# Kernel tuning notes

Hardware: AMD Instinct MI355X
Metric: run time of the kernel (lower is better)

The kernel has to match this reference:

```python
import jax, jax.numpy as jnp
import numpy as np

K = 512   # codebook entries per group (num_embeddings // 4)
D = 128   # dim per group (embedding_dim // 4)
BETA = 0.25


def setup_inputs() -> dict:
    key = jax.random.key(0)
    k0, k1, k2, k3, k4 = jax.random.split(key, 5)
    latents = jax.random.normal(k0, (16, 2048, 512), dtype=jnp.float32)
    scale = 1.0 / K
    w1 = jax.random.uniform(k1, (K, D), dtype=jnp.float32, minval=-scale, maxval=scale)
    w2 = jax.random.uniform(k2, (K, D), dtype=jnp.float32, minval=-scale, maxval=scale)
    w3 = jax.random.uniform(k3, (K, D), dtype=jnp.float32, minval=-scale, maxval=scale)
    w4 = jax.random.uniform(k4, (K, D), dtype=jnp.float32, minval=-scale, maxval=scale)
    return {"latents": latents, "w1": w1, "w2": w2, "w3": w3, "w4": w4}


def _vq(latents, w1, w2, w3, w4):
    B, S, E = latents.shape
    # Slicing [:, :, g*D:(g+1)*D] is equivalent to reshape into groups.
    x = latents.reshape(B, S, 4, D)                    # [B,S,4,D]
    W = jnp.stack([w1, w2, w3, w4], axis=0)            # [4,K,D]
    x_sq = jnp.sum(x * x, axis=-1, keepdims=True)      # [B,S,4,1]
    w_sq = jnp.sum(W * W, axis=-1)                     # [4,K]
    cross = jnp.einsum('bsgd,gkd->bsgk', x, W)         # [B,S,4,K]
    dist = x_sq + w_sq[None, None, :, :] - 2.0 * cross
    idx = jnp.argmin(dist, axis=-1)                    # [B,S,4]
    g_idx = jnp.arange(4)[None, None, :]
    q = W[g_idx, idx]                                  # [B,S,4,D]
    # per-group MSE losses (mean over B,S,D)
    sg = jax.lax.stop_gradient
    commit = jnp.mean((sg(q) - x) ** 2, axis=(0, 1, 3))   # [4]
    embed = jnp.mean((q - sg(x)) ** 2, axis=(0, 1, 3))    # [4]
    vq_loss = jnp.sum(BETA * commit + embed)
    # straight-through estimator
    q_st = x + sg(q - x)
    return q_st.reshape(B, S, E), vq_loss


def reference(latents, w1, w2, w3, w4):
    return _vq(latents, w1, w2, w3, w4)
```

## Files before the change

kernel.cpp:

```cpp
#include <hip/hip_runtime.h>
#include <stdint.h>

typedef __attribute__((ext_vector_type(8))) short short8;
typedef __attribute__((ext_vector_type(4))) float f32x4;

#define BIG 4.0f

static __device__ __forceinline__ short f2bf(float f) {
    union { float f; uint32_t u; } v; v.f = f;
    uint32_t u = v.u;
    return (short)((u + 0x7FFFu + ((u >> 16) & 1u)) >> 16);
}

static __device__ __forceinline__ void gload_lds16(const void* g, void* l) {
    __builtin_amdgcn_global_load_lds(
        (const __attribute__((address_space(1))) unsigned int*)g,
        (__attribute__((address_space(3))) unsigned int*)l, 16, 0, 0);
}


__global__ void vq_prep_kernel(const float* __restrict__ w0, const float* __restrict__ w1,
                               const float* __restrict__ w2, const float* __restrict__ w3,
                               float* __restrict__ ws) {
    int tid = blockIdx.x * 256 + threadIdx.x;
    int code = tid >> 4;
    int u    = tid & 15;
    int g = code >> 9, c = code & 511;
    int nt = c >> 4, lr = c & 15, ks = u >> 2, lh = u & 3;
    const float* wg = (g == 0) ? w0 : (g == 1) ? w1 : (g == 2) ? w2 : w3;
    const float* src = wg + (size_t)c * 128 + u * 8;
    float4 v0 = *(const float4*)(src);
    float4 v1 = *(const float4*)(src + 4);
    float s = v0.x*v0.x + v0.y*v0.y + v0.z*v0.z + v0.w*v0.w
            + v1.x*v1.x + v1.y*v1.y + v1.z*v1.z + v1.w*v1.w;
    short8 b;
    b[0] = f2bf(v0.x); b[1] = f2bf(v0.y); b[2] = f2bf(v0.z); b[3] = f2bf(v0.w);
    b[4] = f2bf(v1.x); b[5] = f2bf(v1.y); b[6] = f2bf(v1.z); b[7] = f2bf(v1.w);
    char* cb = (char*)ws + 65536 + (size_t)g * 131072;
    *(short8*)(cb + (size_t)(((nt * 4 + ks) * 64 + lh * 16 + lr) * 16)) = b;
    s += __shfl_xor(s, 1); s += __shfl_xor(s, 2);
    s += __shfl_xor(s, 4); s += __shfl_xor(s, 8);
    if (u == 0) ws[64 + code] = BIG - 0.5f * s;
}

__global__ __launch_bounds__(512, 2)
void vq_main_kernel(const float* __restrict__ lat,
                    const float* __restrict__ w0, const float* __restrict__ w1,
                    const float* __restrict__ w2, const float* __restrict__ w3,
                    float* __restrict__ out, float* __restrict__ ws) {
    __shared__ __align__(16) short lw[65536];
    __shared__ float lwsq[512];
    __shared__ float slsum[8];

    const int bid   = blockIdx.x;
    const int g     = bid >> 6;
    const int tbase = (bid & 63) * 512;
    const float* wg = (g == 0) ? w0 : (g == 1) ? w1 : (g == 2) ? w2 : w3;
    const char* cbg = (const char*)ws + 65536 + (size_t)g * 131072;

    const int t    = threadIdx.x;
    const int wave = t >> 6;
    const int l    = t & 63;
    const int lr   = l & 15;
    const int lh   = l >> 4;
    const uint32_t invlr = 511 - lr;

    lwsq[t] = ws[64 + g * 512 + t];

    {
        const char* gsrc = cbg + wave * 16384 + l * 16;
        char* ldst = (char*)lw + wave * 16384;
        #pragma unroll
        for (int j = 0; j < 16; j++)
            gload_lds16(gsrc + j * 1024, ldst + j * 1024);
    }

    auto load_convert = [&](short8 (&fr)[2][4], float (&xsp)[2], int wt) {
        #pragma unroll
        for (int mt = 0; mt < 2; mt++) {
            int token = wt + mt * 16 + lr;
            const float* xp = lat + (size_t)token * 512 + g * 128 + lh * 8;
            float part = 0.f;
            #pragma unroll
            for (int ks = 0; ks < 4; ks++) {
                float4 v0 = *(const float4*)(xp + ks * 32);
                float4 v1 = *(const float4*)(xp + ks * 32 + 4);
                part += v0.x*v0.x + v0.y*v0.y + v0.z*v0.z + v0.w*v0.w
                      + v1.x*v1.x + v1.y*v1.y + v1.z*v1.z + v1.w*v1.w;
                short8 a;
                a[0] = f2bf(v0.x); a[1] = f2bf(v0.y); a[2] = f2bf(v0.z); a[3] = f2bf(v0.w);
                a[4] = f2bf(v1.x); a[5] = f2bf(v1.y); a[6] = f2bf(v1.z); a[7] = f2bf(v1.w);
                fr[mt][ks] = a;
            }
            part += __shfl_xor(part, 16);
            part += __shfl_xor(part, 32);
            xsp[mt] = part;
        }
    };

    const char* lwb = (const char*)lw + l * 16;

    auto compute = [&](short8 (&af)[2][4], uint32_t (&rk)[8]) {
        short8 p0 = *(const short8*)(lwb);
        short8 p1 = *(const short8*)(lwb + 1024);
        short8 p2 = *(const short8*)(lwb + 2048);
        short8 p3 = *(const short8*)(lwb + 3072);
        float  ph = lwsq[lr];
        #pragma unroll 4
        for (int nt = 0; nt < 32; nt++) {
            short8 c0 = p0, c1 = p1, c2 = p2, c3 = p3;
            float  hn = ph;
            const char* nb = lwb + ((nt + 1) & 31) * 4096;
            p0 = *(const short8*)(nb);
            p1 = *(const short8*)(nb + 1024);
            p2 = *(const short8*)(nb + 2048);
            p3 = *(const short8*)(nb + 3072);
            ph = lwsq[(((nt + 1) & 31) << 4) + lr];
            const uint32_t invc = invlr - (uint32_t)(nt * 16);
            #pragma unroll
            for (int mt = 0; mt < 2; mt++) {
                f32x4 acc = {hn, hn, hn, hn};
                acc = __builtin_amdgcn_mfma_f32_16x16x32_bf16(af[mt][0], c0, acc, 0, 0, 0);
                acc = __builtin_amdgcn_mfma_f32_16x16x32_bf16(af[mt][1], c1, acc, 0, 0, 0);
                acc = __builtin_amdgcn_mfma_f32_16x16x32_bf16(af[mt][2], c2, acc, 0, 0, 0);
                acc = __builtin_amdgcn_mfma_f32_16x16x32_bf16(af[mt][3], c3, acc, 0, 0, 0);
                #pragma unroll
                for (int r = 0; r < 4; r++) {
                    uint32_t key = (__float_as_uint(acc[r]) & 0xFFFFFE00u) | invc;
                    rk[mt * 4 + r] = max(rk[mt * 4 + r], key);
                }
            }
        }
    };

    auto epilogue = [&](uint32_t (&rk)[8], float (&xsp)[2], int wt, float& acc_lsum) {
        int runidx[8];
        #pragma unroll
        for (int i = 0; i < 8; i++) {
            uint32_t k = rk[i];
            k = max(k, (uint32_t)__shfl_xor((int)k, 1));
            k = max(k, (uint32_t)__shfl_xor((int)k, 2));
            k = max(k, (uint32_t)__shfl_xor((int)k, 4));
            k = max(k, (uint32_t)__shfl_xor((int)k, 8));
            rk[i] = k;
            runidx[i] = 511 - (int)(k & 0x1FFu);
        }
        #pragma unroll
        for (int mt = 0; mt < 2; mt++) {
            #pragma unroll
            for (int r = 0; r < 4; r++) {
                int row = lh * 4 + r;
                float xs = __shfl(xsp[mt], (l & 48) | row);
                float val = __uint_as_float(rk[mt * 4 + r] & 0xFFFFFE00u);
                if (lr == 0) acc_lsum += xs + 2.f * BIG - 2.f * val;
            }
        }
        #pragma unroll
        for (int it = 0; it < 16; it++) {
            const int j0 = it * 2, j1 = it * 2 + 1;
            int idx0 = __shfl(runidx[((j0 >> 4) << 2) | (j0 & 3)], ((j0 >> 2) & 3) << 4);
            int idx1 = __shfl(runidx[((j1 >> 4) << 2) | (j1 & 3)], ((j1 >> 2) & 3) << 4);
            int idx  = (l >= 32) ? idx1 : idx0;
            int tloc = it * 2 + (l >> 5);
            int col  = (l & 31) * 4;
            float4 v = *(const float4*)(wg + (size_t)idx * 128 + col);
            *(float4*)(out + (size_t)(wt + tloc) * 512 + g * 128 + col) = v;
        }
    };

    const int wtok = tbase + wave * 64;

    short8 fA[2][4], fB[2][4];
    float  xspA[2], xspB[2];
    uint32_t kA[8], kB[8];
    #pragma unroll
    for (int i = 0; i < 8; i++) { kA[i] = 0u; kB[i] = 0u; }

    load_convert(fA, xspA, wtok);
    __syncthreads();

    float lsum = 0.f;
    compute(fA, kA);

    float4 raw[16];
    #pragma unroll
    for (int mt = 0; mt < 2; mt++) {
        #pragma unroll
        for (int ks = 0; ks < 4; ks++) {
            const float* xp = lat + (size_t)(wtok + 32 + mt * 16 + lr) * 512
                            + g * 128 + lh * 8 + ks * 32;
            raw[mt * 8 + ks * 2]     = *(const float4*)(xp);
            raw[mt * 8 + ks * 2 + 1] = *(const float4*)(xp + 4);
        }
    }

    epilogue(kA, xspA, wtok, lsum);

    #pragma unroll
    for (int mt = 0; mt < 2; mt++) {
        float part = 0.f;
        #pragma unroll
        for (int ks = 0; ks < 4; ks++) {
            float4 v0 = raw[mt * 8 + ks * 2];
            float4 v1 = raw[mt * 8 + ks * 2 + 1];
            part += v0.x*v0.x + v0.y*v0.y + v0.z*v0.z + v0.w*v0.w
                  + v1.x*v1.x + v1.y*v1.y + v1.z*v1.z + v1.w*v1.w;
            short8 a;
            a[0] = f2bf(v0.x); a[1] = f2bf(v0.y); a[2] = f2bf(v0.z); a[3] = f2bf(v0.w);
            a[4] = f2bf(v1.x); a[5] = f2bf(v1.y); a[6] = f2bf(v1.z); a[7] = f2bf(v1.w);
            fB[mt][ks] = a;
        }
        part += __shfl_xor(part, 16);
        part += __shfl_xor(part, 32);
        xspB[mt] = part;
    }

    compute(fB, kB);
    epilogue(kB, xspB, wtok + 32, lsum);

    lsum += __shfl_xor(lsum, 16);
    lsum += __shfl_xor(lsum, 32);
    if (l == 0) slsum[wave] = lsum;
    __syncthreads();
    if (t == 0) {
        float s = 0.f;
        #pragma unroll
        for (int i = 0; i < 8; i++) s += slsum[i];
        ws[4096 + bid] = s;
    }
}

__global__ void vq_finalize_kernel(const float* __restrict__ ws, float* __restrict__ out) {
    __shared__ float s4[4];
    float v = ws[4096 + threadIdx.x];
    #pragma unroll
    for (int m = 1; m < 64; m <<= 1) v += __shfl_xor(v, m);
    if ((threadIdx.x & 63) == 0) s4[threadIdx.x >> 6] = v;
    __syncthreads();
    if (threadIdx.x == 0)
        out[16777216] = 1.25f * (s4[0] + s4[1] + s4[2] + s4[3]) * (1.0f / 4194304.0f);
}

extern "C" void kernel_launch(void* const* d_in, const int* in_sizes, int n_in,
                              void* d_out, int out_size, void* d_ws, size_t ws_size,
                              hipStream_t stream) {
    const float* lat = (const float*)d_in[0];
    const float* w1  = (const float*)d_in[1];
    const float* w2  = (const float*)d_in[2];
    const float* w3  = (const float*)d_in[3];
    const float* w4  = (const float*)d_in[4];
    float* out = (float*)d_out;
    float* ws  = (float*)d_ws;

    vq_prep_kernel<<<128, 256, 0, stream>>>(w1, w2, w3, w4, ws);
    vq_main_kernel<<<256, 512, 0, stream>>>(lat, w1, w2, w3, w4, out, ws);
    vq_finalize_kernel<<<1, 256, 0, stream>>>(ws, out);
}
```

Baseline: 43.95 us.

## Interleave first tile's codebook gather/store with second tile's MFMA loop

```diff
diff --git a/kernel.cpp b/kernel.cpp
--- a/kernel.cpp
+++ b/kernel.cpp
@@ -63,6 +63,7 @@
     const int l    = t & 63;
     const int lr   = l & 15;
     const int lh   = l >> 4;
+    const int col  = (l & 31) * 4;
     const uint32_t invlr = 511 - lr;
 
     lwsq[t] = ws[64 + g * 512 + t];
@@ -117,18 +118,22 @@
             p3 = *(const short8*)(nb + 3072);
             ph = lwsq[(((nt + 1) & 31) << 4) + lr];
             const uint32_t invc = invlr - (uint32_t)(nt * 16);
+            __builtin_amdgcn_s_setprio(1);
+            f32x4 acc0 = {hn, hn, hn, hn};
+            f32x4 acc1 = {hn, hn, hn, hn};
+            acc0 = __builtin_amdgcn_mfma_f32_16x16x32_bf16(af[0][0], c0, acc0, 0, 0, 0);
+            acc0 = __builtin_amdgcn_mfma_f32_16x16x32_bf16(af[0][1], c1, acc0, 0, 0, 0);
+            acc0 = __builtin_amdgcn_mfma_f32_16x16x32_bf16(af[0][2], c2, acc0, 0, 0, 0);
+            acc0 = __builtin_amdgcn_mfma_f32_16x16x32_bf16(af[0][3], c3, acc0, 0, 0, 0);
+            acc1 = __builtin_amdgcn_mfma_f32_16x16x32_bf16(af[1][0], c0, acc1, 0, 0, 0);
+            acc1 = __builtin_amdgcn_mfma_f32_16x16x32_bf16(af[1][1], c1, acc1, 0, 0, 0);
+            acc1 = __builtin_amdgcn_mfma_f32_16x16x32_bf16(af[1][2], c2, acc1, 0, 0, 0);
+            acc1 = __builtin_amdgcn_mfma_f32_16x16x32_bf16(af[1][3], c3, acc1, 0, 0, 0);
+            __builtin_amdgcn_s_setprio(0);
             #pragma unroll
-            for (int mt = 0; mt < 2; mt++) {
-                f32x4 acc = {hn, hn, hn, hn};
-                acc = __builtin_amdgcn_mfma_f32_16x16x32_bf16(af[mt][0], c0, acc, 0, 0, 0);
-                acc = __builtin_amdgcn_mfma_f32_16x16x32_bf16(af[mt][1], c1, acc, 0, 0, 0);
-                acc = __builtin_amdgcn_mfma_f32_16x16x32_bf16(af[mt][2], c2, acc, 0, 0, 0);
-                acc = __builtin_amdgcn_mfma_f32_16x16x32_bf16(af[mt][3], c3, acc, 0, 0, 0);
-                #pragma unroll
-                for (int r = 0; r < 4; r++) {
-                    uint32_t key = (__float_as_uint(acc[r]) & 0xFFFFFE00u) | invc;
-                    rk[mt * 4 + r] = max(rk[mt * 4 + r], key);
-                }
+            for (int r = 0; r < 4; r++) {
+                rk[r]     = max(rk[r],     (__float_as_uint(acc0[r]) & 0xFFFFFE00u) | invc);
+                rk[4 + r] = max(rk[4 + r], (__float_as_uint(acc1[r]) & 0xFFFFFE00u) | invc);
             }
         }
     };
@@ -162,7 +167,6 @@
             int idx1 = __shfl(runidx[((j1 >> 4) << 2) | (j1 & 3)], ((j1 >> 2) & 3) << 4);
             int idx  = (l >= 32) ? idx1 : idx0;
             int tloc = it * 2 + (l >> 5);
-            int col  = (l & 31) * 4;
             float4 v = *(const float4*)(wg + (size_t)idx * 128 + col);
             *(float4*)(out + (size_t)(wt + tloc) * 512 + g * 128 + col) = v;
         }
@@ -194,7 +198,35 @@
         }
     }
 
-    epilogue(kA, xspA, wtok, lsum);
+    int runidxA[8];
+    #pragma unroll
+    for (int i = 0; i < 8; i++) {
+        uint32_t k = kA[i];
+        k = max(k, (uint32_t)__shfl_xor((int)k, 1));
+        k = max(k, (uint32_t)__shfl_xor((int)k, 2));
+        k = max(k, (uint32_t)__shfl_xor((int)k, 4));
+        k = max(k, (uint32_t)__shfl_xor((int)k, 8));
+        kA[i] = k;
+        runidxA[i] = 511 - (int)(k & 0x1FFu);
+    }
+    #pragma unroll
+    for (int mt = 0; mt < 2; mt++) {
+        #pragma unroll
+        for (int r = 0; r < 4; r++) {
+            int row = lh * 4 + r;
+            float xs = __shfl(xspA[mt], (l & 48) | row);
+            float val = __uint_as_float(kA[mt * 4 + r] & 0xFFFFFE00u);
+            if (lr == 0) lsum += xs + 2.f * BIG - 2.f * val;
+        }
+    }
+    int widx[16];
+    #pragma unroll
+    for (int it = 0; it < 16; it++) {
+        const int j0 = it * 2, j1 = it * 2 + 1;
+        int idx0 = __shfl(runidxA[((j0 >> 4) << 2) | (j0 & 3)], ((j0 >> 2) & 3) << 4);
+        int idx1 = __shfl(runidxA[((j1 >> 4) << 2) | (j1 & 3)], ((j1 >> 2) & 3) << 4);
+        widx[it] = (l >= 32) ? idx1 : idx0;
+    }
 
     #pragma unroll
     for (int mt = 0; mt < 2; mt++) {
@@ -215,7 +247,65 @@
         xspB[mt] = part;
     }
 
-    compute(fB, kB);
+    {
+        short8 p0 = *(const short8*)(lwb);
+        short8 p1 = *(const short8*)(lwb + 1024);
+        short8 p2 = *(const short8*)(lwb + 2048);
+        short8 p3 = *(const short8*)(lwb + 3072);
+        float  ph = lwsq[lr];
+        float4 vb0, vb1;
+
+#define FUSED_NT(nt)                                                           \
+        {                                                                      \
+            short8 c0 = p0, c1 = p1, c2 = p2, c3 = p3;                         \
+            float  hn = ph;                                                    \
+            const char* nb = lwb + (((nt) + 1) & 31) * 4096;                   \
+            p0 = *(const short8*)(nb);                                         \
+            p1 = *(const short8*)(nb + 1024);                                  \
+            p2 = *(const short8*)(nb + 2048);                                  \
+            p3 = *(const short8*)(nb + 3072);                                  \
+            ph = lwsq[((((nt) + 1) & 31) << 4) + lr];                          \
+            const uint32_t invc = invlr - (uint32_t)((nt) * 16);               \
+            __builtin_amdgcn_s_setprio(1);                                     \
+            f32x4 acc0 = {hn, hn, hn, hn};                                     \
+            f32x4 acc1 = {hn, hn, hn, hn};                                     \
+            acc0 = __builtin_amdgcn_mfma_f32_16x16x32_bf16(fB[0][0], c0, acc0, 0, 0, 0); \
+            acc0 = __builtin_amdgcn_mfma_f32_16x16x32_bf16(fB[0][1], c1, acc0, 0, 0, 0); \
+            acc0 = __builtin_amdgcn_mfma_f32_16x16x32_bf16(fB[0][2], c2, acc0, 0, 0, 0); \
+            acc0 = __builtin_amdgcn_mfma_f32_16x16x32_bf16(fB[0][3], c3, acc0, 0, 0, 0); \
+            acc1 = __builtin_amdgcn_mfma_f32_16x16x32_bf16(fB[1][0], c0, acc1, 0, 0, 0); \
+            acc1 = __builtin_amdgcn_mfma_f32_16x16x32_bf16(fB[1][1], c1, acc1, 0, 0, 0); \
+            acc1 = __builtin_amdgcn_mfma_f32_16x16x32_bf16(fB[1][2], c2, acc1, 0, 0, 0); \
+            acc1 = __builtin_amdgcn_mfma_f32_16x16x32_bf16(fB[1][3], c3, acc1, 0, 0, 0); \
+            __builtin_amdgcn_s_setprio(0);                                     \
+            kB[0] = max(kB[0], (__float_as_uint(acc0[0]) & 0xFFFFFE00u) | invc); \
+            kB[1] = max(kB[1], (__float_as_uint(acc0[1]) & 0xFFFFFE00u) | invc); \
+            kB[2] = max(kB[2], (__float_as_uint(acc0[2]) & 0xFFFFFE00u) | invc); \
+            kB[3] = max(kB[3], (__float_as_uint(acc0[3]) & 0xFFFFFE00u) | invc); \
+            kB[4] = max(kB[4], (__float_as_uint(acc1[0]) & 0xFFFFFE00u) | invc); \
+            kB[5] = max(kB[5], (__float_as_uint(acc1[1]) & 0xFFFFFE00u) | invc); \
+            kB[6] = max(kB[6], (__float_as_uint(acc1[2]) & 0xFFFFFE00u) | invc); \
+            kB[7] = max(kB[7], (__float_as_uint(acc1[3]) & 0xFFFFFE00u) | invc); \
+            if (((nt) & 3) == 1) {                                             \
+                const int it0 = ((nt) >> 2) * 2;                               \
+                vb0 = *(const float4*)(wg + (size_t)widx[it0] * 128 + col);    \
+                vb1 = *(const float4*)(wg + (size_t)widx[it0 + 1] * 128 + col);\
+            }                                                                  \
+            if (((nt) & 3) == 3) {                                             \
+                const int it0 = ((nt) >> 2) * 2;                               \
+                *(float4*)(out + (size_t)(wtok + it0 * 2 + (l >> 5)) * 512     \
+                           + g * 128 + col) = vb0;                             \
+                *(float4*)(out + (size_t)(wtok + (it0 + 1) * 2 + (l >> 5)) * 512 \
+                           + g * 128 + col) = vb1;                             \
+            }                                                                  \
+        }
+#define FUSED_4(n) FUSED_NT(n) FUSED_NT((n) + 1) FUSED_NT((n) + 2) FUSED_NT((n) + 3)
+        FUSED_4(0)  FUSED_4(4)  FUSED_4(8)  FUSED_4(12)
+        FUSED_4(16) FUSED_4(20) FUSED_4(24) FUSED_4(28)
+#undef FUSED_4
+#undef FUSED_NT
+    }
+
     epilogue(kB, xspB, wtok + 32, lsum);
 
     lsum += __shfl_xor(lsum, 16);
```

Result: faster. 40.43 us (-8.0%).
